# Kernel tuning notes

Hardware: AMD Instinct MI355X
Metric: run time of the kernel (lower is better)

## Reference

```python
import jax, jax.numpy as jnp
import numpy as np

N, F, H, O = 16384, 64, 128, 512

def setup_inputs() -> dict:
    key = jax.random.key(0)
    ks = jax.random.split(key, 5)
    # PyTorch Linear default init: U(-1/sqrt(fan_in), 1/sqrt(fan_in))
    lim1 = 1.0  # fan_in = 1 for Linear(1, H)
    lim2 = 1.0 / np.sqrt(H)
    x = jax.random.normal(ks[0], (N, F), dtype=jnp.float32)
    W1 = jax.random.uniform(ks[1], (F, H), minval=-lim1, maxval=lim1, dtype=jnp.float32)
    b1 = jax.random.uniform(ks[2], (F, H), minval=-lim1, maxval=lim1, dtype=jnp.float32)
    W2 = jax.random.uniform(ks[3], (F, H, O), minval=-lim2, maxval=lim2, dtype=jnp.float32)
    b2 = jax.random.uniform(ks[4], (F, O), minval=-lim2, maxval=lim2, dtype=jnp.float32)
    return {"x": x, "W1": W1, "b1": b1, "W2": W2, "b2": b2}

def reference(x, W1, b1, W2, b2):
    # Per-feature MLP: h_f = W2_f @ elu(x_f * w1_f + b1_f) + b2_f, summed over f.
    # pre: [N, F, H] = outer-product of each scalar feature with its W1 row
    pre = x[:, :, None] * W1[None, :, :] + b1[None, :, :]
    a = jax.nn.elu(pre)                                  # [N, F, H]
    h = jnp.einsum('nfh,fho->no', a, W2)                 # sum over f and h
    h = h + jnp.sum(b2, axis=0)[None, :]                 # biases summed over F
    return h / jnp.sqrt(jnp.float32(F))
```

## Files before the change

kernel.cpp:

```cpp
#include <hip/hip_runtime.h>
#include <cstdint>

#define NROWS 16384
#define FDIM 64
#define HDIM 128
#define ODIM 512
#define KDIM 8192

#define BM 64
#define BN 256
#define BK 64
#define NST 128

typedef short bf16x8 __attribute__((ext_vector_type(8)));
typedef float f32x4 __attribute__((ext_vector_type(4)));
typedef uint32_t u32x4 __attribute__((ext_vector_type(4)));

__device__ __forceinline__ uint16_t rne_bf16(float f) {
  uint32_t u = __builtin_bit_cast(uint32_t, f);
  u += 0x7fffu + ((u >> 16) & 1u);
  return (uint16_t)(u >> 16);
}

__global__ void prep_w2t(const float* __restrict__ W2, uint16_t* __restrict__ W2T) {
  __shared__ float tile[64][65];
  const int k0 = blockIdx.x * 64;
  const int o0 = blockIdx.y * 64;
  const int tx = threadIdx.x;
  const int ty = threadIdx.y;
#pragma unroll
  for (int j = 0; j < 8; ++j)
    tile[ty + 8 * j][tx] = W2[(size_t)(k0 + ty + 8 * j) * ODIM + o0 + tx];
  __syncthreads();
#pragma unroll
  for (int j = 0; j < 8; ++j)
    W2T[(size_t)(o0 + ty + 8 * j) * KDIM + k0 + tx] = rne_bf16(tile[tx][ty + 8 * j]);
}

__global__ void prep_small(const float* __restrict__ W1, const float* __restrict__ b1,
                           const float* __restrict__ b2, uint16_t* __restrict__ w1bf,
                           uint16_t* __restrict__ b1bf, float* __restrict__ b2sum) {
  const int t = blockIdx.x * 256 + threadIdx.x;
  w1bf[t] = rne_bf16(W1[t]);
  b1bf[t] = rne_bf16(b1[t]);
  if (t < ODIM) {
    float s = 0.f;
#pragma unroll
    for (int f = 0; f < FDIM; ++f) s += b2[(size_t)f * ODIM + t];
    b2sum[t] = s;
  }
}

struct Pref {
  u32x4 w1d, b1d;
  float xv0, xv1;
};

__global__ __launch_bounds__(256, 2) void mlp_gemm(
    const float* __restrict__ x, const uint16_t* __restrict__ w1bf,
    const uint16_t* __restrict__ b1bf, const uint16_t* __restrict__ W2T,
    const float* __restrict__ b2sum, float* __restrict__ out) {
  __shared__ __align__(16) uint16_t As0[BM * BK];
  __shared__ __align__(16) uint16_t As1[BM * BK];
  __shared__ __align__(16) uint16_t Bs0[BN * BK];
  __shared__ __align__(16) uint16_t Bs1[BN * BK];

  const int tid = threadIdx.x;
  const int bid = blockIdx.x;
  const int o0 = (bid & 1) * BN;
  const int m0 = (bid >> 1) * BM;

  const int wid = tid >> 6;
  const int lane = tid & 63;
  const int wn = wid * 64;
  const int q = lane >> 4;
  const int r = lane & 15;

  const int ar = tid >> 3;
  const int ac = tid & 7;
  const int brow = lane >> 3;
  const int bcg = (lane & 7) ^ brow;

  f32x4 acc[4][4];
#pragma unroll
  for (int i = 0; i < 4; ++i)
#pragma unroll
    for (int j = 0; j < 4; ++j) acc[i][j] = {0.f, 0.f, 0.f, 0.f};

  auto ldops = [&](Pref& P, int s) {
    const int f = s >> 1;
    const int hoff = (s & 1) * 64 + ac * 8;
    P.w1d = *(const u32x4*)(w1bf + f * HDIM + hoff);
    P.b1d = *(const u32x4*)(b1bf + f * HDIM + hoff);
    P.xv0 = x[(size_t)(m0 + ar) * FDIM + f];
    P.xv1 = x[(size_t)(m0 + 32 + ar) * FDIM + f];
  };

  auto stageB = [&](uint16_t* Bb, int kk) {
#pragma unroll
    for (int j = 0; j < 8; ++j) {
      const int chunk = wid * 8 + j;
      const uint16_t* gp =
          W2T + (size_t)(o0 + chunk * 8 + brow) * KDIM + kk * BK + bcg * 8;
      uint16_t* lp = Bb + chunk * 512;
      __builtin_amdgcn_global_load_lds(
          (const __attribute__((address_space(1))) uint32_t*)gp,
          (__attribute__((address_space(3))) uint32_t*)lp, 16, 0, 0);
    }
  };

  auto eluA = [&](uint16_t* Ab, const Pref& P) {
    float w1f[8], b1f[8];
#pragma unroll
    for (int p = 0; p < 4; ++p) {
      w1f[2 * p]     = __builtin_bit_cast(float, P.w1d[p] << 16);
      w1f[2 * p + 1] = __builtin_bit_cast(float, P.w1d[p] & 0xffff0000u);
      b1f[2 * p]     = __builtin_bit_cast(float, P.b1d[p] << 16);
      b1f[2 * p + 1] = __builtin_bit_cast(float, P.b1d[p] & 0xffff0000u);
    }
#pragma unroll
    for (int i = 0; i < 2; ++i) {
      const float xv = i ? P.xv1 : P.xv0;
      const int m = i * 32 + ar;
      u32x4 ov;
#pragma unroll
      for (int p = 0; p < 4; ++p) {
        float plo = fmaf(xv, w1f[2 * p], b1f[2 * p]);
        float phi = fmaf(xv, w1f[2 * p + 1], b1f[2 * p + 1]);
        float elo = plo > 0.f ? plo : __expf(plo) - 1.f;
        float ehi = phi > 0.f ? phi : __expf(phi) - 1.f;
        ov[p] = __builtin_amdgcn_perm(__builtin_bit_cast(uint32_t, ehi),
                                      __builtin_bit_cast(uint32_t, elo),
                                      0x07060302u);
      }
      *(u32x4*)&Ab[m * BK + ((ac ^ (m & 7)) * 8)] = ov;
    }
  };

  auto compute = [&](const uint16_t* Ab, const uint16_t* Bb) {
#pragma unroll
    for (int kc = 0; kc < 2; ++kc) {
      bf16x8 af[4], bfr[4];
      const int cg = kc * 4 + q;
#pragma unroll
      for (int mt = 0; mt < 4; ++mt) {
        const int row = mt * 16 + r;
        af[mt] = *(const bf16x8*)&Ab[row * BK + ((cg ^ (row & 7)) * 8)];
      }
#pragma unroll
      for (int nt = 0; nt < 4; ++nt) {
        const int row = wn + nt * 16 + r;
        bfr[nt] = *(const bf16x8*)&Bb[row * BK + ((cg ^ (row & 7)) * 8)];
      }
#pragma unroll
      for (int mt = 0; mt < 4; ++mt)
#pragma unroll
        for (int nt = 0; nt < 4; ++nt)
          acc[mt][nt] = __builtin_amdgcn_mfma_f32_16x16x32_bf16(
              af[mt], bfr[nt], acc[mt][nt], 0, 0, 0);
    }
  };

  Pref P0, P1;

  ldops(P0, 0);
  __builtin_amdgcn_sched_barrier(0);
  stageB(Bs0, 0);
  eluA(As0, P0);
  ldops(P1, 1);
  __syncthreads();

#pragma unroll 1
  for (int kk = 0; kk < NST - 2; kk += 2) {
    ldops(P0, kk + 2);
    __builtin_amdgcn_sched_barrier(0);
    stageB(Bs1, kk + 1);
    eluA(As1, P1);
    compute(As0, Bs0);
    __syncthreads();
    ldops(P1, kk + 3);
    __builtin_amdgcn_sched_barrier(0);
    stageB(Bs0, kk + 2);
    eluA(As0, P0);
    compute(As1, Bs1);
    __syncthreads();
  }
  stageB(Bs1, NST - 1);
  eluA(As1, P1);
  compute(As0, Bs0);
  __syncthreads();
  compute(As1, Bs1);

  float bsv[4];
#pragma unroll
  for (int nt = 0; nt < 4; ++nt) bsv[nt] = b2sum[o0 + wn + nt * 16 + r];
#pragma unroll
  for (int mt = 0; mt < 4; ++mt)
#pragma unroll
    for (int nt = 0; nt < 4; ++nt)
#pragma unroll
      for (int v = 0; v < 4; ++v) {
        const int row = m0 + mt * 16 + q * 4 + v;
        const int col = o0 + wn + nt * 16 + r;
        out[(size_t)row * ODIM + col] = (acc[mt][nt][v] + bsv[nt]) * 0.125f;
      }
}

extern "C" void kernel_launch(void* const* d_in, const int* in_sizes, int n_in,
                              void* d_out, int out_size, void* d_ws, size_t ws_size,
                              hipStream_t stream) {
  const float* x  = (const float*)d_in[0];
  const float* W1 = (const float*)d_in[1];
  const float* b1 = (const float*)d_in[2];
  const float* W2 = (const float*)d_in[3];
  const float* b2 = (const float*)d_in[4];
  float* out = (float*)d_out;

  char* ws = (char*)d_ws;
  float*    b2sum = (float*)ws;
  uint16_t* w1bf  = (uint16_t*)(ws + 4096);
  uint16_t* b1bf  = (uint16_t*)(ws + 4096 + 16384);
  uint16_t* W2T   = (uint16_t*)(ws + 65536);

  prep_w2t<<<dim3(KDIM / 64, ODIM / 64), dim3(64, 8), 0, stream>>>(W2, W2T);
  prep_small<<<32, 256, 0, stream>>>(W1, b1, b2, w1bf, b1bf, b2sum);
  mlp_gemm<<<(NROWS / BM) * (ODIM / BN), 256, 0, stream>>>(x, w1bf, b1bf, W2T,
                                                           b2sum, out);
}
```

Baseline: 252.8 us.

## Cover full output width per block and drop the small prep kernel

Each GEMM block now spans all 512 output columns using 8 waves, where before two 256-column blocks shared each row tile. The ELU activation tile is now computed once per row tile instead of twice, and each thread handles one row rather than two. W1 and b1 are read directly as fp32, which removes their bf16 conversion. The b2 sum moves into the W2 transpose kernel, so there is one fewer launch. LDS use grows to about 144KB per block, so only one block fits per CU, and the grid halves to 256 blocks.

```diff
diff --git a/kernel.cpp b/kernel.cpp
--- a/kernel.cpp
+++ b/kernel.cpp
@@ -8,7 +8,7 @@
 #define KDIM 8192
 
 #define BM 64
-#define BN 256
+#define BN 512
 #define BK 64
 #define NST 128
 
@@ -22,7 +22,8 @@
   return (uint16_t)(u >> 16);
 }
 
-__global__ void prep_w2t(const float* __restrict__ W2, uint16_t* __restrict__ W2T) {
+__global__ void prep_w2t(const float* __restrict__ W2, uint16_t* __restrict__ W2T,
+                         const float* __restrict__ b2, float* __restrict__ b2sum) {
   __shared__ float tile[64][65];
   const int k0 = blockIdx.x * 64;
   const int o0 = blockIdx.y * 64;
@@ -35,30 +36,23 @@
 #pragma unroll
   for (int j = 0; j < 8; ++j)
     W2T[(size_t)(o0 + ty + 8 * j) * KDIM + k0 + tx] = rne_bf16(tile[tx][ty + 8 * j]);
-}
-
-__global__ void prep_small(const float* __restrict__ W1, const float* __restrict__ b1,
-                           const float* __restrict__ b2, uint16_t* __restrict__ w1bf,
-                           uint16_t* __restrict__ b1bf, float* __restrict__ b2sum) {
-  const int t = blockIdx.x * 256 + threadIdx.x;
-  w1bf[t] = rne_bf16(W1[t]);
-  b1bf[t] = rne_bf16(b1[t]);
-  if (t < ODIM) {
+  if (blockIdx.x == 0 && blockIdx.y == 0) {
+    const int o = ty * 64 + tx;
     float s = 0.f;
 #pragma unroll
-    for (int f = 0; f < FDIM; ++f) s += b2[(size_t)f * ODIM + t];
-    b2sum[t] = s;
+    for (int f = 0; f < FDIM; ++f) s += b2[(size_t)f * ODIM + o];
+    b2sum[o] = s;
   }
 }
 
 struct Pref {
-  u32x4 w1d, b1d;
-  float xv0, xv1;
+  f32x4 wlo, whi, blo, bhi;
+  float xv;
 };
 
-__global__ __launch_bounds__(256, 2) void mlp_gemm(
-    const float* __restrict__ x, const uint16_t* __restrict__ w1bf,
-    const uint16_t* __restrict__ b1bf, const uint16_t* __restrict__ W2T,
+__global__ __launch_bounds__(512, 2) void mlp_gemm(
+    const float* __restrict__ x, const float* __restrict__ W1,
+    const float* __restrict__ b1, const uint16_t* __restrict__ W2T,
     const float* __restrict__ b2sum, float* __restrict__ out) {
   __shared__ __align__(16) uint16_t As0[BM * BK];
   __shared__ __align__(16) uint16_t As1[BM * BK];
@@ -66,9 +60,7 @@
   __shared__ __align__(16) uint16_t Bs1[BN * BK];
 
   const int tid = threadIdx.x;
-  const int bid = blockIdx.x;
-  const int o0 = (bid & 1) * BN;
-  const int m0 = (bid >> 1) * BM;
+  const int m0 = blockIdx.x * BM;
 
   const int wid = tid >> 6;
   const int lane = tid & 63;
@@ -78,6 +70,7 @@
 
   const int ar = tid >> 3;
   const int ac = tid & 7;
+  const int awc = (ac ^ (ar & 7)) * 8;
   const int brow = lane >> 3;
   const int bcg = (lane & 7) ^ brow;
 
@@ -90,10 +83,13 @@
   auto ldops = [&](Pref& P, int s) {
     const int f = s >> 1;
     const int hoff = (s & 1) * 64 + ac * 8;
-    P.w1d = *(const u32x4*)(w1bf + f * HDIM + hoff);
-    P.b1d = *(const u32x4*)(b1bf + f * HDIM + hoff);
-    P.xv0 = x[(size_t)(m0 + ar) * FDIM + f];
-    P.xv1 = x[(size_t)(m0 + 32 + ar) * FDIM + f];
+    const float* wp = W1 + (size_t)f * HDIM + hoff;
+    const float* bp = b1 + (size_t)f * HDIM + hoff;
+    P.wlo = *(const f32x4*)wp;
+    P.whi = *(const f32x4*)(wp + 4);
+    P.blo = *(const f32x4*)bp;
+    P.bhi = *(const f32x4*)(bp + 4);
+    P.xv = x[(size_t)(m0 + ar) * FDIM + f];
   };
 
   auto stageB = [&](uint16_t* Bb, int kk) {
@@ -101,7 +97,7 @@
     for (int j = 0; j < 8; ++j) {
       const int chunk = wid * 8 + j;
       const uint16_t* gp =
-          W2T + (size_t)(o0 + chunk * 8 + brow) * KDIM + kk * BK + bcg * 8;
+          W2T + (size_t)(chunk * 8 + brow) * KDIM + kk * BK + bcg * 8;
       uint16_t* lp = Bb + chunk * 512;
       __builtin_amdgcn_global_load_lds(
           (const __attribute__((address_space(1))) uint32_t*)gp,
@@ -110,31 +106,22 @@
   };
 
   auto eluA = [&](uint16_t* Ab, const Pref& P) {
-    float w1f[8], b1f[8];
+    u32x4 ov;
 #pragma unroll
     for (int p = 0; p < 4; ++p) {
-      w1f[2 * p]     = __builtin_bit_cast(float, P.w1d[p] << 16);
-      w1f[2 * p + 1] = __builtin_bit_cast(float, P.w1d[p] & 0xffff0000u);
-      b1f[2 * p]     = __builtin_bit_cast(float, P.b1d[p] << 16);
-      b1f[2 * p + 1] = __builtin_bit_cast(float, P.b1d[p] & 0xffff0000u);
+      const float we0 = (p < 2) ? P.wlo[2 * p] : P.whi[2 * p - 4];
+      const float we1 = (p < 2) ? P.wlo[2 * p + 1] : P.whi[2 * p - 3];
+      const float be0 = (p < 2) ? P.blo[2 * p] : P.bhi[2 * p - 4];
+      const float be1 = (p < 2) ? P.blo[2 * p + 1] : P.bhi[2 * p - 3];
+      float plo = fmaf(P.xv, we0, be0);
+      float phi = fmaf(P.xv, we1, be1);
+      float elo = plo > 0.f ? plo : __expf(plo) - 1.f;
+      float ehi = phi > 0.f ? phi : __expf(phi) - 1.f;
+      ov[p] = __builtin_amdgcn_perm(__builtin_bit_cast(uint32_t, ehi),
+                                    __builtin_bit_cast(uint32_t, elo),
+                                    0x07060302u);
     }
-#pragma unroll
-    for (int i = 0; i < 2; ++i) {
-      const float xv = i ? P.xv1 : P.xv0;
-      const int m = i * 32 + ar;
-      u32x4 ov;
-#pragma unroll
-      for (int p = 0; p < 4; ++p) {
-        float plo = fmaf(xv, w1f[2 * p], b1f[2 * p]);
-        float phi = fmaf(xv, w1f[2 * p + 1], b1f[2 * p + 1]);
-        float elo = plo > 0.f ? plo : __expf(plo) - 1.f;
-        float ehi = phi > 0.f ? phi : __expf(phi) - 1.f;
-        ov[p] = __builtin_amdgcn_perm(__builtin_bit_cast(uint32_t, ehi),
-                                      __builtin_bit_cast(uint32_t, elo),
-                                      0x07060302u);
-      }
-      *(u32x4*)&Ab[m * BK + ((ac ^ (m & 7)) * 8)] = ov;
-    }
+    *(u32x4*)&Ab[ar * BK + awc] = ov;
   };
 
   auto compute = [&](const uint16_t* Ab, const uint16_t* Bb) {
@@ -193,7 +180,7 @@
 
   float bsv[4];
 #pragma unroll
-  for (int nt = 0; nt < 4; ++nt) bsv[nt] = b2sum[o0 + wn + nt * 16 + r];
+  for (int nt = 0; nt < 4; ++nt) bsv[nt] = b2sum[wn + nt * 16 + r];
 #pragma unroll
   for (int mt = 0; mt < 4; ++mt)
 #pragma unroll
@@ -201,7 +188,7 @@
 #pragma unroll
       for (int v = 0; v < 4; ++v) {
         const int row = m0 + mt * 16 + q * 4 + v;
-        const int col = o0 + wn + nt * 16 + r;
+        const int col = wn + nt * 16 + r;
         out[(size_t)row * ODIM + col] = (acc[mt][nt][v] + bsv[nt]) * 0.125f;
       }
 }
@@ -218,12 +205,8 @@
 
   char* ws = (char*)d_ws;
   float*    b2sum = (float*)ws;
-  uint16_t* w1bf  = (uint16_t*)(ws + 4096);
-  uint16_t* b1bf  = (uint16_t*)(ws + 4096 + 16384);
   uint16_t* W2T   = (uint16_t*)(ws + 65536);
 
-  prep_w2t<<<dim3(KDIM / 64, ODIM / 64), dim3(64, 8), 0, stream>>>(W2, W2T);
-  prep_small<<<32, 256, 0, stream>>>(W1, b1, b2, w1bf, b1bf, b2sum);
-  mlp_gemm<<<(NROWS / BM) * (ODIM / BN), 256, 0, stream>>>(x, w1bf, b1bf, W2T,
-                                                           b2sum, out);
-}
+  prep_w2t<<<dim3(KDIM / 64, ODIM / 64), dim3(64, 8), 0, stream>>>(W2, W2T, b2, b2sum);
+  mlp_gemm<<<NROWS / BM, 512, 0, stream>>>(x, W1, b1, W2T, b2sum, out);
+}
```

Result: faster. 230.0 us (-9.0%).
